# Kernel optimization log

Hardware: AMD Instinct MI355X
Metric: run time of the kernel (lower is better)

Reference implementation:

```python
import jax, jax.numpy as jnp
import numpy as np

N = 4096      # nodes
F = 128       # input feature dim
HEADS = 8     # attention_num
U = 8         # units per head


def setup_inputs() -> dict:
    key = jax.random.key(0)
    k_a, k_h, k_w, k_al, k_ar = jax.random.split(key, 5)
    A = jax.random.randint(k_a, (N, N), 0, 2).astype(jnp.float32)   # dense 0/1 adjacency
    H = jax.random.normal(k_h, (N, F), dtype=jnp.float32)
    W = jax.random.normal(k_w, (HEADS, F, U), dtype=jnp.float32) * 0.1
    a_left = jax.random.normal(k_al, (HEADS, U), dtype=jnp.float32) * 0.1
    a_right = jax.random.normal(k_ar, (HEADS, U), dtype=jnp.float32) * 0.1
    return {"A": A, "H": H, "W": W, "a_left": a_left, "a_right": a_right}


def reference(A, H, W, a_left, a_right):
    # Per-head attention logits: E[h,i,j] = e_left[h,i] + e_right[h,j]
    e_l = jnp.einsum('nf,hfu,hu->hn', H, W, a_left)    # [HEADS, N]
    e_r = jnp.einsum('nf,hfu,hu->hn', H, W, a_right)   # [HEADS, N]
    E = e_l[:, :, None] + e_r[:, None, :]              # [HEADS, N, N]
    # Faithful to original: denominator uses exp(E * A) (zeros in A -> exp(0)=1)
    denom = jnp.sum(jnp.exp(E * A[None]), axis=-1, keepdims=True)   # [HEADS, N, 1]
    Alpha = jnp.exp(E) / denom * A[None]               # masked attention weights
    # Aggregate then project: elu(Alpha @ H @ W) per head
    out = jax.nn.elu(jnp.einsum('hij,jf,hfu->hiu', Alpha, H, W))    # [HEADS, N, U]
    # is_output_layer=False -> concat heads along feature dim: [N, HEADS*U]
    return jnp.transpose(out, (1, 0, 2)).reshape(H.shape[0], HEADS * U)
```

## Files before the change

### kernel.cpp

```cpp
#include <hip/hip_runtime.h>
#include <hip/hip_bf16.h>

#define NN 4096
#define FF 128
#define NC 80
#define LSTR 84

typedef __attribute__((ext_vector_type(4))) float float4v;
typedef __attribute__((ext_vector_type(4))) unsigned int uint4v;
typedef __attribute__((ext_vector_type(8))) short short8;

static __device__ inline unsigned short bfb(float x) {
    __hip_bfloat16 b = __float2bfloat16(x);
    return *(unsigned short*)&b;
}
static __device__ inline float bff(unsigned short u) {
    __hip_bfloat16 b = *(__hip_bfloat16*)&u;
    return __bfloat162float(b);
}

__global__ __launch_bounds__(256) void gat_wsplit(const float* __restrict__ W,
                                                  const float* __restrict__ al,
                                                  const float* __restrict__ ar,
                                                  __hip_bfloat16* __restrict__ Wphi,
                                                  __hip_bfloat16* __restrict__ Wplo)
{
    const int tid = blockIdx.x * 256 + threadIdx.x;
    if (tid >= 80 * FF) return;
    const int c = tid % 80;
    const int f = tid / 80;
    float val;
    if (c < 64) {
        val = W[(size_t)(c >> 3) * (FF * 8) + (size_t)f * 8 + (c & 7)];
    } else {
        const int hc = (c - 64) & 7;
        const float* ap = (c < 72) ? ar : al;
        const float* wp = W + (size_t)hc * (FF * 8) + (size_t)f * 8;
        float s = 0.f;
        #pragma unroll
        for (int u = 0; u < 8; ++u) s += wp[u] * ap[hc * 8 + u];
        val = s;
    }
    const unsigned short h = bfb(val);
    const unsigned short l = bfb(val - bff(h));
    const int g = (f >> 5) * 4 + ((f >> 3) & 3);
    const size_t idx = ((size_t)g * NC + c) * 8 + (f & 7);
    Wphi[idx] = *(const __hip_bfloat16*)&h;
    Wplo[idx] = *(const __hip_bfloat16*)&l;
}

__global__ __launch_bounds__(256) void gat_prep(const float* __restrict__ H,
                                                const __hip_bfloat16* __restrict__ Wphi,
                                                const __hip_bfloat16* __restrict__ Wplo,
                                                float* __restrict__ expEl,
                                                __hip_bfloat16* __restrict__ Bp)
{
    __shared__ float Lp[4 * 16 * LSTR];
    const int t    = threadIdx.x;
    const int wave = t >> 6;
    const int lane = t & 63;
    const int j0   = blockIdx.x * 16;
    const int m16  = lane & 15, q = lane >> 4;
    const short* Whs = (const short*)Wphi;
    const short* Wls = (const short*)Wplo;
    const int kt = wave;

    const float* hp = H + (size_t)(j0 + m16) * FF + kt * 32 + q * 8;
    float4v x0 = *(const float4v*)hp;
    float4v x1 = *(const float4v*)(hp + 4);
    short8 ahi, alo;
    #pragma unroll
    for (int i = 0; i < 4; ++i) {
        const unsigned short h0 = bfb(x0[i]);
        ahi[i] = (short)h0;
        alo[i] = (short)bfb(x0[i] - bff(h0));
        const unsigned short h1 = bfb(x1[i]);
        ahi[4 + i] = (short)h1;
        alo[4 + i] = (short)bfb(x1[i] - bff(h1));
    }

    const short8* bh = (const short8*)(Whs + (size_t)(kt * 4 + q) * NC * 8);
    const short8* bl = (const short8*)(Wls + (size_t)(kt * 4 + q) * NC * 8);
    float4v acc[5] = {};
    #pragma unroll
    for (int nt = 0; nt < 5; ++nt) {
        short8 bhi = bh[nt * 16 + m16];
        short8 blo = bl[nt * 16 + m16];
        acc[nt] = __builtin_amdgcn_mfma_f32_16x16x32_bf16(ahi, bhi, acc[nt], 0, 0, 0);
        acc[nt] = __builtin_amdgcn_mfma_f32_16x16x32_bf16(alo, bhi, acc[nt], 0, 0, 0);
        acc[nt] = __builtin_amdgcn_mfma_f32_16x16x32_bf16(ahi, blo, acc[nt], 0, 0, 0);
    }

    float* Lw = Lp + wave * (16 * LSTR);
    #pragma unroll
    for (int nt = 0; nt < 5; ++nt) {
        #pragma unroll
        for (int r = 0; r < 4; ++r)
            Lw[(q * 4 + r) * LSTR + nt * 16 + m16] = acc[nt][r];
    }
    __syncthreads();

    const int jl = t >> 4, g = t & 15;
    const float* Lr = Lp + jl * LSTR;
    const int jg = j0 + jl;
    const size_t base = ((size_t)((jg >> 5) * 4 + ((jg >> 3) & 3)) * NC) * 8 + (jg & 7);

    #pragma unroll
    for (int i = 0; i < 4; ++i) {
        const int c = g + 16 * i;
        const int h = (g >> 3) + 2 * i;
        const float er = expf(Lr[64 + h] + Lr[16 * LSTR + 64 + h] +
                              Lr[32 * LSTR + 64 + h] + Lr[48 * LSTR + 64 + h]);
        const float v = Lr[c] + Lr[16 * LSTR + c] +
                        Lr[32 * LSTR + c] + Lr[48 * LSTR + c];
        Bp[base + (size_t)c * 8] = __float2bfloat16(er * v);
    }
    float v64;
    if (g < 8) {
        v64 = expf(Lr[64 + g] + Lr[16 * LSTR + 64 + g] +
                   Lr[32 * LSTR + 64 + g] + Lr[48 * LSTR + 64 + g]);
    } else {
        v64 = (g == 8) ? 1.0f : 0.0f;
    }
    Bp[base + (size_t)(64 + g) * 8] = __float2bfloat16(v64);
    if (g >= 8) {
        const int h = g - 8;
        expEl[h * NN + jg] = expf(Lr[72 + h] + Lr[16 * LSTR + 72 + h] +
                                  Lr[32 * LSTR + 72 + h] + Lr[48 * LSTR + 72 + h]);
    }
}

__global__ __launch_bounds__(512) void gat_gemm(const float* __restrict__ A,
                                                const __hip_bfloat16* __restrict__ Bp,
                                                const float* __restrict__ expEl,
                                                float* __restrict__ out)
{
    __shared__ float Ls[8 * 16 * LSTR];
    const int rb   = blockIdx.x;
    const int wave = threadIdx.x >> 6;
    const int lane = threadIdx.x & 63;
    const int m16  = lane & 15;
    const int q    = lane >> 4;
    const int row0 = rb * 16;

    float4v acc[5] = {};

    const int k0 = wave * 512;
    const unsigned int* Au = (const unsigned int*)A;
    const short* Bs = (const short*)Bp;
    const unsigned int* arow = Au + (size_t)(row0 + m16) * NN + q * 8 + k0;

    uint4v a0[2], a1[2];
    a0[0] = *(const uint4v*)(arow);      a1[0] = *(const uint4v*)(arow + 4);
    a0[1] = *(const uint4v*)(arow + 32); a1[1] = *(const uint4v*)(arow + 36);

    #pragma unroll
    for (int kt = 0; kt < 16; ++kt) {
        const int cur = kt & 1;
        short8 afrag;
        afrag[0] = (short)(a0[cur][0] >> 16); afrag[1] = (short)(a0[cur][1] >> 16);
        afrag[2] = (short)(a0[cur][2] >> 16); afrag[3] = (short)(a0[cur][3] >> 16);
        afrag[4] = (short)(a1[cur][0] >> 16); afrag[5] = (short)(a1[cur][1] >> 16);
        afrag[6] = (short)(a1[cur][2] >> 16); afrag[7] = (short)(a1[cur][3] >> 16);

        if (kt + 2 < 16) {
            a0[cur] = *(const uint4v*)(arow + (kt + 2) * 32);
            a1[cur] = *(const uint4v*)(arow + (kt + 2) * 32 + 4);
        }

        const int ktg = (k0 >> 5) + kt;
        const short8* bbase = (const short8*)(Bs + ((size_t)(ktg * 4 + q) * NC) * 8);
        #pragma unroll
        for (int nt = 0; nt < 5; ++nt) {
            short8 bfrag = bbase[nt * 16 + m16];
            acc[nt] = __builtin_amdgcn_mfma_f32_16x16x32_bf16(afrag, bfrag, acc[nt], 0, 0, 0);
        }
    }

    float* Lw = Ls + wave * (16 * LSTR);
    #pragma unroll
    for (int nt = 0; nt < 5; ++nt) {
        #pragma unroll
        for (int r = 0; r < 4; ++r)
            Lw[(q * 4 + r) * LSTR + nt * 16 + m16] = acc[nt][r];
    }
    __syncthreads();

    #pragma unroll
    for (int p = threadIdx.x; p < 1024; p += 512) {
        const int il = p >> 6;
        const int c  = p & 63;
        const int h  = c >> 3;
        float T = 0.f, S = 0.f, dg = 0.f;
        #pragma unroll
        for (int w = 0; w < 8; ++w) {
            const float* rowp = Ls + w * (16 * LSTR) + il * LSTR;
            T  += rowp[c];
            S  += rowp[64 + h];
            dg += rowp[72];
        }
        const float el = expEl[h * NN + row0 + il];
        const float denom = ((float)NN - dg) + el * S;
        const float x = el * T / denom;
        out[(size_t)(row0 + il) * 64 + c] = x > 0.f ? x : expf(x) - 1.f;
    }
}

extern "C" void kernel_launch(void* const* d_in, const int* in_sizes, int n_in,
                              void* d_out, int out_size, void* d_ws, size_t ws_size,
                              hipStream_t stream) {
    const float* A  = (const float*)d_in[0];
    const float* H  = (const float*)d_in[1];
    const float* W  = (const float*)d_in[2];
    const float* al = (const float*)d_in[3];
    const float* ar = (const float*)d_in[4];
    float* out = (float*)d_out;

    float* expEl = (float*)d_ws;
    __hip_bfloat16* Bp   = (__hip_bfloat16*)((char*)d_ws + 131072);
    __hip_bfloat16* Wphi = (__hip_bfloat16*)((char*)d_ws + 131072 + 655360);
    __hip_bfloat16* Wplo = (__hip_bfloat16*)((char*)d_ws + 131072 + 655360 + 20480);

    gat_wsplit<<<40, 256, 0, stream>>>(W, al, ar, Wphi, Wplo);
    gat_prep<<<NN / 16, 256, 0, stream>>>(H, Wphi, Wplo, expEl, Bp);
    gat_gemm<<<NN / 16, 512, 0, stream>>>(A, Bp, expEl, out);
}
```

Measured before the change: 118.4 us.

## Fuse W split into prep kernel and widen GEMM split-K to 16 waves

Removes the separate gat_wsplit launch: each gat_prep block now computes the bf16 hi/lo split of W and the attention projection vectors into shared memory before its MFMA step. This saves one kernel launch and a global round trip, at the cost of 256 blocks redundantly recomputing the same small W transform. Separately, gat_gemm now runs 1024 threads (16 waves) per block, each covering a 256-wide K slice instead of 512. This adds memory-level parallelism for streaming A but doubles the shared-memory reduction buffer and the reduction work.

```diff
diff --git a/kernel.cpp b/kernel.cpp
--- a/kernel.cpp
+++ b/kernel.cpp
@@ -9,6 +9,7 @@
 typedef __attribute__((ext_vector_type(4))) float float4v;
 typedef __attribute__((ext_vector_type(4))) unsigned int uint4v;
 typedef __attribute__((ext_vector_type(8))) short short8;
+typedef __attribute__((ext_vector_type(8))) unsigned short ushort8;
 
 static __device__ inline unsigned short bfb(float x) {
     __hip_bfloat16 b = __float2bfloat16(x);
@@ -19,84 +20,97 @@
     return __bfloat162float(b);
 }
 
-__global__ __launch_bounds__(256) void gat_wsplit(const float* __restrict__ W,
-                                                  const float* __restrict__ al,
-                                                  const float* __restrict__ ar,
-                                                  __hip_bfloat16* __restrict__ Wphi,
-                                                  __hip_bfloat16* __restrict__ Wplo)
-{
-    const int tid = blockIdx.x * 256 + threadIdx.x;
-    if (tid >= 80 * FF) return;
-    const int c = tid % 80;
-    const int f = tid / 80;
-    float val;
-    if (c < 64) {
-        val = W[(size_t)(c >> 3) * (FF * 8) + (size_t)f * 8 + (c & 7)];
-    } else {
-        const int hc = (c - 64) & 7;
-        const float* ap = (c < 72) ? ar : al;
-        const float* wp = W + (size_t)hc * (FF * 8) + (size_t)f * 8;
-        float s = 0.f;
-        #pragma unroll
-        for (int u = 0; u < 8; ++u) s += wp[u] * ap[hc * 8 + u];
-        val = s;
-    }
-    const unsigned short h = bfb(val);
-    const unsigned short l = bfb(val - bff(h));
-    const int g = (f >> 5) * 4 + ((f >> 3) & 3);
-    const size_t idx = ((size_t)g * NC + c) * 8 + (f & 7);
-    Wphi[idx] = *(const __hip_bfloat16*)&h;
-    Wplo[idx] = *(const __hip_bfloat16*)&l;
-}
-
 __global__ __launch_bounds__(256) void gat_prep(const float* __restrict__ H,
-                                                const __hip_bfloat16* __restrict__ Wphi,
-                                                const __hip_bfloat16* __restrict__ Wplo,
+                                                const float* __restrict__ W,
+                                                const float* __restrict__ al,
+                                                const float* __restrict__ ar,
                                                 float* __restrict__ expEl,
                                                 __hip_bfloat16* __restrict__ Bp)
 {
+    __shared__ unsigned short Whi[16 * NC * 8], Wlo[16 * NC * 8];
     __shared__ float Lp[4 * 16 * LSTR];
-    const int t    = threadIdx.x;
-    const int wave = t >> 6;
-    const int lane = t & 63;
-    const int j0   = blockIdx.x * 16;
-    const int m16  = lane & 15, q = lane >> 4;
-    const short* Whs = (const short*)Wphi;
-    const short* Wls = (const short*)Wplo;
-    const int kt = wave;
-
-    const float* hp = H + (size_t)(j0 + m16) * FF + kt * 32 + q * 8;
-    float4v x0 = *(const float4v*)hp;
-    float4v x1 = *(const float4v*)(hp + 4);
-    short8 ahi, alo;
-    #pragma unroll
-    for (int i = 0; i < 4; ++i) {
-        const unsigned short h0 = bfb(x0[i]);
-        ahi[i] = (short)h0;
-        alo[i] = (short)bfb(x0[i] - bff(h0));
-        const unsigned short h1 = bfb(x1[i]);
-        ahi[4 + i] = (short)h1;
-        alo[4 + i] = (short)bfb(x1[i] - bff(h1));
-    }
-
-    const short8* bh = (const short8*)(Whs + (size_t)(kt * 4 + q) * NC * 8);
-    const short8* bl = (const short8*)(Wls + (size_t)(kt * 4 + q) * NC * 8);
-    float4v acc[5] = {};
-    #pragma unroll
-    for (int nt = 0; nt < 5; ++nt) {
-        short8 bhi = bh[nt * 16 + m16];
-        short8 blo = bl[nt * 16 + m16];
-        acc[nt] = __builtin_amdgcn_mfma_f32_16x16x32_bf16(ahi, bhi, acc[nt], 0, 0, 0);
-        acc[nt] = __builtin_amdgcn_mfma_f32_16x16x32_bf16(alo, bhi, acc[nt], 0, 0, 0);
-        acc[nt] = __builtin_amdgcn_mfma_f32_16x16x32_bf16(ahi, blo, acc[nt], 0, 0, 0);
-    }
-
-    float* Lw = Lp + wave * (16 * LSTR);
-    #pragma unroll
-    for (int nt = 0; nt < 5; ++nt) {
-        #pragma unroll
-        for (int r = 0; r < 4; ++r)
-            Lw[(q * 4 + r) * LSTR + nt * 16 + m16] = acc[nt][r];
+    const int t  = threadIdx.x;
+    const int j0 = blockIdx.x * 16;
+
+    {
+        const int hu = t & 63;
+        const int fb = (t >> 6) * 32;
+        const float* wsrc = W + (size_t)(hu >> 3) * (FF * 8) + (hu & 7);
+        #pragma unroll
+        for (int g8 = 0; g8 < 4; ++g8) {
+            const int f0 = fb + g8 * 8;
+            ushort8 hv, lv;
+            #pragma unroll
+            for (int i = 0; i < 8; ++i) {
+                float x = wsrc[(size_t)(f0 + i) * 8];
+                unsigned short h = bfb(x);
+                hv[i] = h; lv[i] = bfb(x - bff(h));
+            }
+            const int g = (f0 >> 5) * 4 + ((f0 >> 3) & 3);
+            *(ushort8*)&Whi[((size_t)g * NC + hu) * 8] = hv;
+            *(ushort8*)&Wlo[((size_t)g * NC + hu) * 8] = lv;
+        }
+    }
+    {
+        const int h  = t >> 5;
+        const int f0 = (t & 31) * 4;
+        float arv[8], alv[8];
+        #pragma unroll
+        for (int u = 0; u < 8; ++u) { arv[u] = ar[h * 8 + u]; alv[u] = al[h * 8 + u]; }
+        #pragma unroll
+        for (int i = 0; i < 4; ++i) {
+            const int f = f0 + i;
+            const float* wp = W + (size_t)h * (FF * 8) + (size_t)f * 8;
+            float sr = 0.f, sl = 0.f;
+            #pragma unroll
+            for (int u = 0; u < 8; ++u) { float w = wp[u]; sr += w * arv[u]; sl += w * alv[u]; }
+            const int g = (f >> 5) * 4 + ((f >> 3) & 3);
+            unsigned short a = bfb(sr);
+            Whi[((size_t)g * NC + 64 + h) * 8 + (f & 7)] = a;
+            Wlo[((size_t)g * NC + 64 + h) * 8 + (f & 7)] = bfb(sr - bff(a));
+            unsigned short b = bfb(sl);
+            Whi[((size_t)g * NC + 72 + h) * 8 + (f & 7)] = b;
+            Wlo[((size_t)g * NC + 72 + h) * 8 + (f & 7)] = bfb(sl - bff(b));
+        }
+    }
+    __syncthreads();
+
+    {
+        const int wave = t >> 6, lane = t & 63;
+        const int m16 = lane & 15, q = lane >> 4;
+        const int kt = wave;
+
+        const float* hp = H + (size_t)(j0 + m16) * FF + kt * 32 + q * 8;
+        float4v x0 = *(const float4v*)hp;
+        float4v x1 = *(const float4v*)(hp + 4);
+        short8 ahi, alo;
+        #pragma unroll
+        for (int i = 0; i < 4; ++i) {
+            const unsigned short h0 = bfb(x0[i]);
+            ahi[i] = (short)h0;
+            alo[i] = (short)bfb(x0[i] - bff(h0));
+            const unsigned short h1 = bfb(x1[i]);
+            ahi[4 + i] = (short)h1;
+            alo[4 + i] = (short)bfb(x1[i] - bff(h1));
+        }
+
+        float4v acc[5] = {};
+        #pragma unroll
+        for (int nt = 0; nt < 5; ++nt) {
+            short8 bhi = *(const short8*)&Whi[((size_t)(kt * 4 + q) * NC + nt * 16 + m16) * 8];
+            short8 blo = *(const short8*)&Wlo[((size_t)(kt * 4 + q) * NC + nt * 16 + m16) * 8];
+            acc[nt] = __builtin_amdgcn_mfma_f32_16x16x32_bf16(ahi, bhi, acc[nt], 0, 0, 0);
+            acc[nt] = __builtin_amdgcn_mfma_f32_16x16x32_bf16(alo, bhi, acc[nt], 0, 0, 0);
+            acc[nt] = __builtin_amdgcn_mfma_f32_16x16x32_bf16(ahi, blo, acc[nt], 0, 0, 0);
+        }
+
+        float* Lw = Lp + wave * (16 * LSTR);
+        #pragma unroll
+        for (int nt = 0; nt < 5; ++nt) {
+            #pragma unroll
+            for (int r = 0; r < 4; ++r)
+                Lw[(q * 4 + r) * LSTR + nt * 16 + m16] = acc[nt][r];
+        }
     }
     __syncthreads();
 
@@ -130,12 +144,12 @@
     }
 }
 
-__global__ __launch_bounds__(512) void gat_gemm(const float* __restrict__ A,
-                                                const __hip_bfloat16* __restrict__ Bp,
-                                                const float* __restrict__ expEl,
-                                                float* __restrict__ out)
+__global__ __launch_bounds__(1024) void gat_gemm(const float* __restrict__ A,
+                                                 const __hip_bfloat16* __restrict__ Bp,
+                                                 const float* __restrict__ expEl,
+                                                 float* __restrict__ out)
 {
-    __shared__ float Ls[8 * 16 * LSTR];
+    __shared__ float Ls[16 * 16 * LSTR];
     const int rb   = blockIdx.x;
     const int wave = threadIdx.x >> 6;
     const int lane = threadIdx.x & 63;
@@ -145,7 +159,7 @@
 
     float4v acc[5] = {};
 
-    const int k0 = wave * 512;
+    const int k0 = wave * 256;
     const unsigned int* Au = (const unsigned int*)A;
     const short* Bs = (const short*)Bp;
     const unsigned int* arow = Au + (size_t)(row0 + m16) * NN + q * 8 + k0;
@@ -155,7 +169,7 @@
     a0[1] = *(const uint4v*)(arow + 32); a1[1] = *(const uint4v*)(arow + 36);
 
     #pragma unroll
-    for (int kt = 0; kt < 16; ++kt) {
+    for (int kt = 0; kt < 8; ++kt) {
         const int cur = kt & 1;
         short8 afrag;
         afrag[0] = (short)(a0[cur][0] >> 16); afrag[1] = (short)(a0[cur][1] >> 16);
@@ -163,12 +177,12 @@
         afrag[4] = (short)(a1[cur][0] >> 16); afrag[5] = (short)(a1[cur][1] >> 16);
         afrag[6] = (short)(a1[cur][2] >> 16); afrag[7] = (short)(a1[cur][3] >> 16);
 
-        if (kt + 2 < 16) {
+        if (kt + 2 < 8) {
             a0[cur] = *(const uint4v*)(arow + (kt + 2) * 32);
             a1[cur] = *(const uint4v*)(arow + (kt + 2) * 32 + 4);
         }
 
-        const int ktg = (k0 >> 5) + kt;
+        const int ktg = wave * 8 + kt;
         const short8* bbase = (const short8*)(Bs + ((size_t)(ktg * 4 + q) * NC) * 8);
         #pragma unroll
         for (int nt = 0; nt < 5; ++nt) {
@@ -186,14 +200,14 @@
     }
     __syncthreads();
 
-    #pragma unroll
-    for (int p = threadIdx.x; p < 1024; p += 512) {
+    {
+        const int p  = threadIdx.x;
         const int il = p >> 6;
         const int c  = p & 63;
         const int h  = c >> 3;
         float T = 0.f, S = 0.f, dg = 0.f;
         #pragma unroll
-        for (int w = 0; w < 8; ++w) {
+        for (int w = 0; w < 16; ++w) {
             const float* rowp = Ls + w * (16 * LSTR) + il * LSTR;
             T  += rowp[c];
             S  += rowp[64 + h];
@@ -217,11 +231,8 @@
     float* out = (float*)d_out;
 
     float* expEl = (float*)d_ws;
-    __hip_bfloat16* Bp   = (__hip_bfloat16*)((char*)d_ws + 131072);
-    __hip_bfloat16* Wphi = (__hip_bfloat16*)((char*)d_ws + 131072 + 655360);
-    __hip_bfloat16* Wplo = (__hip_bfloat16*)((char*)d_ws + 131072 + 655360 + 20480);
-
-    gat_wsplit<<<40, 256, 0, stream>>>(W, al, ar, Wphi, Wplo);
-    gat_prep<<<NN / 16, 256, 0, stream>>>(H, Wphi, Wplo, expEl, Bp);
-    gat_gemm<<<NN / 16, 512, 0, stream>>>(A, Bp, expEl, out);
-}
+    __hip_bfloat16* Bp = (__hip_bfloat16*)((char*)d_ws + 131072);
+
+    gat_prep<<<NN / 16, 256, 0, stream>>>(H, W, al, ar, expEl, Bp);
+    gat_gemm<<<NN / 16, 1024, 0, stream>>>(A, Bp, expEl, out);
+}
```

New measurement: 117.6 us. Within noise of the previous version (-0.7%).
